# Performance work log

Measured on AMD Instinct MI355X. Metric: run time of the kernel, lower is better.

The kernel has to match this reference:

```python
import jax, jax.numpy as jnp
import numpy as np

RADIUS = 0.05      # outer ball-query radius
MIN_RADIUS = 0.02  # inner exclusion radius


def setup_inputs() -> dict:
    key = jax.random.key(0)
    k1, k2 = jax.random.split(key)
    # raw layout is [B, C, N, 1] as consumed by forward's squeeze(-1).permute(0,2,1)
    xyz = jax.random.uniform(k1, (4, 3, 4096, 1), dtype=jnp.float32)      # coords in unit cube
    points = jax.random.normal(k2, (4, 64, 4096, 1), dtype=jnp.float32)   # per-point features
    return {"xyz": xyz, "points": points}


def _pairwise_sqdist(x):
    # x: [B, N, 3] -> [B, N, N] squared euclidean distances
    sq = jnp.sum(x * x, axis=-1)  # [B, N]
    return sq[:, :, None] + sq[:, None, :] - 2.0 * jnp.einsum('bnc,bmc->bnm', x, x)


def reference(xyz, points):
    # [B, C, N, 1] -> [B, N, C]
    _xyz = jnp.transpose(xyz[..., 0], (0, 2, 1))       # [B, N, 3]
    _points = jnp.transpose(points[..., 0], (0, 2, 1))  # [B, N, D]
    B, N, C = _xyz.shape

    # downsample_query_ball: ball-query neighbor counts in annulus (min_radius, radius),
    # keep the N//2 densest points
    d2 = _pairwise_sqdist(_xyz)                              # [B, N, N]
    nbr_cnt = jnp.sum(((d2 < RADIUS ** 2) & (d2 > MIN_RADIUS ** 2)).astype(jnp.int32), axis=-1)
    _, idx = jax.lax.top_k(nbr_cnt, N // 2)                  # [B, N//2]

    # index_points: gather along the point axis
    new_xyz = jnp.take_along_axis(_xyz, idx[..., None], axis=1)        # [B, N//2, 3]
    new_points = jnp.take_along_axis(_points, idx[..., None], axis=1)  # [B, N//2, D]
    return new_xyz, new_points
```

## Files before the change

### kernel.cpp

```cpp
#include <hip/hip_runtime.h>


#define BN 4
#define NPTS 4096
#define ND 64
#define KSEL 2048
#define R2 0.0025f
#define M2 0.0004f

#define IPT 4
#define ITILES 4
#define JC 32
#define JCH 128

__global__ __launch_bounds__(256) void prep_kernel(
        const float* __restrict__ xyz, float4* __restrict__ pts4,
        int* __restrict__ counts, int* __restrict__ ranks) {
    int tid = blockIdx.x * 256 + threadIdx.x;
    int b = tid >> 12, i = tid & (NPTS - 1);
    const float* base = xyz + (size_t)b * 3 * NPTS;
    float x = base[i], y = base[NPTS + i], z = base[2 * NPTS + i];
    float sq = __fadd_rn(__fadd_rn(__fmul_rn(x, x), __fmul_rn(y, y)),
                         __fmul_rn(z, z));
    pts4[tid] = make_float4(x, y, z, sq);
    counts[tid] = 0;
    ranks[tid] = 0;
}

__global__ __launch_bounds__(256) void count_kernel(
        const float4* __restrict__ pts4, int* __restrict__ counts) {
    __shared__ float4 sj[JCH];
    const int jc = blockIdx.x & (JC - 1);
    const int it = (blockIdx.x >> 5) & (ITILES - 1);
    const int b  = blockIdx.x >> 7;
    const float4* pb = pts4 + b * NPTS;

    if (threadIdx.x < JCH) sj[threadIdx.x] = pb[jc * JCH + threadIdx.x];

    const int ibase = it * 1024 + threadIdx.x;
    float4 mi[IPT];
    #pragma unroll
    for (int k = 0; k < IPT; ++k) mi[k] = pb[ibase + k * 256];
    __syncthreads();

    int cnt[IPT] = {0, 0, 0, 0};
    #pragma unroll 2
    for (int j = 0; j < JCH; ++j) {
        float4 p = sj[j];
        #pragma unroll
        for (int k = 0; k < IPT; ++k) {
            float dot = __fadd_rn(__fadd_rn(__fmul_rn(mi[k].x, p.x),
                                            __fmul_rn(mi[k].y, p.y)),
                                  __fmul_rn(mi[k].z, p.z));
            float d2 = __fsub_rn(__fadd_rn(mi[k].w, p.w), __fmul_rn(2.0f, dot));
            cnt[k] += (d2 < R2 && d2 > M2) ? 1 : 0;
        }
    }
    #pragma unroll
    for (int k = 0; k < IPT; ++k)
        atomicAdd(&counts[b * NPTS + ibase + k * 256], cnt[k]);
}

__global__ __launch_bounds__(256) void rank_kernel(
        const int* __restrict__ counts, int* __restrict__ ranks) {
    __shared__ int skey[JCH];
    const int jc = blockIdx.x & (JC - 1);
    const int it = (blockIdx.x >> 5) & (ITILES - 1);
    const int b  = blockIdx.x >> 7;
    const int* cb = counts + b * NPTS;

    if (threadIdx.x < JCH) {
        int j = jc * JCH + threadIdx.x;
        skey[threadIdx.x] = (cb[j] << 12) | (NPTS - 1 - j);
    }
    const int ibase = it * 1024 + threadIdx.x;
    int ki[IPT];
    #pragma unroll
    for (int k = 0; k < IPT; ++k) {
        int i = ibase + k * 256;
        ki[k] = (cb[i] << 12) | (NPTS - 1 - i);
    }
    __syncthreads();

    int r[IPT] = {0, 0, 0, 0};
    #pragma unroll 2
    for (int j = 0; j < JCH; ++j) {
        int kj = skey[j];
        #pragma unroll
        for (int k = 0; k < IPT; ++k) r[k] += (kj > ki[k]) ? 1 : 0;
    }
    #pragma unroll
    for (int k = 0; k < IPT; ++k)
        atomicAdd(&ranks[b * NPTS + ibase + k * 256], r[k]);
}

__global__ __launch_bounds__(256) void scatter_kernel(
        const float4* __restrict__ pts4, const int* __restrict__ ranks,
        int* __restrict__ sel, float* __restrict__ out) {
    int tid = blockIdx.x * 256 + threadIdx.x;
    int b = tid >> 12, i = tid & (NPTS - 1);
    int r = ranks[tid];
    if (r < KSEL) {
        sel[b * KSEL + r] = i;
        float4 p = pts4[tid];
        float* o = out + (size_t)(b * KSEL + r) * 3;
        o[0] = p.x; o[1] = p.y; o[2] = p.z;
    }
}

__global__ __launch_bounds__(256) void gatherf_kernel(
        const float* __restrict__ points, const int* __restrict__ sel,
        float* __restrict__ out) {
    int flat = blockIdx.x * 256 + threadIdx.x;
    int c = flat & (ND - 1);
    int k = (flat >> 6) & (KSEL - 1);
    int b = flat >> 17;
    int i = sel[b * KSEL + k];
    out[(size_t)BN * KSEL * 3 + flat] =
        points[(size_t)(b * ND + c) * NPTS + i];
}

extern "C" void kernel_launch(void* const* d_in, const int* in_sizes, int n_in,
                              void* d_out, int out_size, void* d_ws, size_t ws_size,
                              hipStream_t stream) {
    const float* xyz    = (const float*)d_in[0];
    const float* points = (const float*)d_in[1];
    float* out = (float*)d_out;

    char* ws = (char*)d_ws;
    float4* pts4 = (float4*)ws;
    int* counts  = (int*)(ws + 256 * 1024);
    int* ranks   = (int*)(ws + 320 * 1024);
    int* sel     = (int*)(ws + 384 * 1024);

    prep_kernel<<<BN * NPTS / 256, 256, 0, stream>>>(xyz, pts4, counts, ranks);
    count_kernel<<<BN * ITILES * JC, 256, 0, stream>>>(pts4, counts);
    rank_kernel<<<BN * ITILES * JC, 256, 0, stream>>>(counts, ranks);
    scatter_kernel<<<BN * NPTS / 256, 256, 0, stream>>>(pts4, ranks, sel, out);
    gatherf_kernel<<<BN * KSEL * ND / 256, 256, 0, stream>>>(points, sel, out);
}
```

Measured before the change: 91.79 us.

## Fuse prep into counting, replace atomics with partials, fuse rank with gather

Removes the prep kernel by computing squared norms inline in the counting kernel. Per-block partial counts are written to a buffer and summed by a small key kernel, replacing atomicAdd and the zero-initialisation. The tiled rank kernel, scatter and feature gather become one kernel that holds all keys in shared memory, computes each point's rank and scatters its coordinates and features directly. This cuts five launches to three and drops the sel indirection, at the cost of only 256 blocks for the rank stage and scattered feature writes.

After: 91.43 us. Within noise of the previous version (-0.4%).

```diff
diff --git a/kernel.cpp b/kernel.cpp
--- a/kernel.cpp
+++ b/kernel.cpp
@@ -13,38 +13,35 @@
 #define JC 32
 #define JCH 128
 
-__global__ __launch_bounds__(256) void prep_kernel(
-        const float* __restrict__ xyz, float4* __restrict__ pts4,
-        int* __restrict__ counts, int* __restrict__ ranks) {
-    int tid = blockIdx.x * 256 + threadIdx.x;
-    int b = tid >> 12, i = tid & (NPTS - 1);
-    const float* base = xyz + (size_t)b * 3 * NPTS;
-    float x = base[i], y = base[NPTS + i], z = base[2 * NPTS + i];
-    float sq = __fadd_rn(__fadd_rn(__fmul_rn(x, x), __fmul_rn(y, y)),
-                         __fmul_rn(z, z));
-    pts4[tid] = make_float4(x, y, z, sq);
-    counts[tid] = 0;
-    ranks[tid] = 0;
-}
-
-__global__ __launch_bounds__(256) void count_kernel(
-        const float4* __restrict__ pts4, int* __restrict__ counts) {
+__global__ __launch_bounds__(256) void count_part_kernel(
+        const float* __restrict__ xyz, int* __restrict__ part) {
     __shared__ float4 sj[JCH];
     const int jc = blockIdx.x & (JC - 1);
     const int it = (blockIdx.x >> 5) & (ITILES - 1);
     const int b  = blockIdx.x >> 7;
-    const float4* pb = pts4 + b * NPTS;
+    const float* base = xyz + (size_t)b * 3 * NPTS;
 
-    if (threadIdx.x < JCH) sj[threadIdx.x] = pb[jc * JCH + threadIdx.x];
-
+    if (threadIdx.x < JCH) {
+        int j = jc * JCH + threadIdx.x;
+        float x = base[j], y = base[NPTS + j], z = base[2 * NPTS + j];
+        float sq = __fadd_rn(__fadd_rn(__fmul_rn(x, x), __fmul_rn(y, y)),
+                             __fmul_rn(z, z));
+        sj[threadIdx.x] = make_float4(x, y, z, sq);
+    }
     const int ibase = it * 1024 + threadIdx.x;
     float4 mi[IPT];
     #pragma unroll
-    for (int k = 0; k < IPT; ++k) mi[k] = pb[ibase + k * 256];
+    for (int k = 0; k < IPT; ++k) {
+        int i = ibase + k * 256;
+        float x = base[i], y = base[NPTS + i], z = base[2 * NPTS + i];
+        float sq = __fadd_rn(__fadd_rn(__fmul_rn(x, x), __fmul_rn(y, y)),
+                             __fmul_rn(z, z));
+        mi[k] = make_float4(x, y, z, sq);
+    }
     __syncthreads();
 
     int cnt[IPT] = {0, 0, 0, 0};
-    #pragma unroll 2
+    #pragma unroll 4
     for (int j = 0; j < JCH; ++j) {
         float4 p = sj[j];
         #pragma unroll
@@ -56,68 +53,64 @@
             cnt[k] += (d2 < R2 && d2 > M2) ? 1 : 0;
         }
     }
+    int* pp = part + (size_t)((b * ITILES + it) * JC + jc) * 1024;
     #pragma unroll
-    for (int k = 0; k < IPT; ++k)
-        atomicAdd(&counts[b * NPTS + ibase + k * 256], cnt[k]);
+    for (int k = 0; k < IPT; ++k) pp[threadIdx.x + k * 256] = cnt[k];
 }
 
-__global__ __launch_bounds__(256) void rank_kernel(
-        const int* __restrict__ counts, int* __restrict__ ranks) {
-    __shared__ int skey[JCH];
-    const int jc = blockIdx.x & (JC - 1);
-    const int it = (blockIdx.x >> 5) & (ITILES - 1);
-    const int b  = blockIdx.x >> 7;
-    const int* cb = counts + b * NPTS;
+__global__ __launch_bounds__(256) void key_kernel(
+        const int* __restrict__ part, int* __restrict__ key) {
+    int tid = blockIdx.x * 256 + threadIdx.x;
+    int b = tid >> 12, i = tid & (NPTS - 1);
+    int it = i >> 10, local = i & 1023;
+    const int* pp = part + (size_t)(b * ITILES + it) * JC * 1024 + local;
+    int c = 0;
+    #pragma unroll
+    for (int jc = 0; jc < JC; ++jc) c += pp[jc * 1024];
+    key[tid] = (c << 12) | (NPTS - 1 - i);
+}
 
-    if (threadIdx.x < JCH) {
-        int j = jc * JCH + threadIdx.x;
-        skey[threadIdx.x] = (cb[j] << 12) | (NPTS - 1 - j);
-    }
-    const int ibase = it * 1024 + threadIdx.x;
-    int ki[IPT];
-    #pragma unroll
-    for (int k = 0; k < IPT; ++k) {
-        int i = ibase + k * 256;
-        ki[k] = (cb[i] << 12) | (NPTS - 1 - i);
+__global__ __launch_bounds__(256) void rank_gather_kernel(
+        const float* __restrict__ xyz, const float* __restrict__ points,
+        const int* __restrict__ key, float* __restrict__ out) {
+    __shared__ int skey[NPTS];
+    __shared__ int spr[4][64];
+    __shared__ int srank[64];
+    const int b     = blockIdx.x >> 6;
+    const int tbase = (blockIdx.x & 63) * 64;
+    const int* kb = key + b * NPTS;
+    for (int idx = threadIdx.x; idx < NPTS; idx += 256) skey[idx] = kb[idx];
+    __syncthreads();
+
+    const int ii = threadIdx.x & 63;
+    const int q  = threadIdx.x >> 6;
+    const int ki = skey[tbase + ii];
+    int r = 0;
+    #pragma unroll 8
+    for (int j = q * 1024; j < q * 1024 + 1024; ++j)
+        r += (skey[j] > ki) ? 1 : 0;
+    spr[q][ii] = r;
+    __syncthreads();
+
+    if (threadIdx.x < 64) {
+        int rank = spr[0][threadIdx.x] + spr[1][threadIdx.x] +
+                   spr[2][threadIdx.x] + spr[3][threadIdx.x];
+        srank[threadIdx.x] = rank;
+        int i = tbase + threadIdx.x;
+        if (rank < KSEL) {
+            const float* xb = xyz + (size_t)b * 3 * NPTS;
+            float* o = out + ((size_t)b * KSEL + rank) * 3;
+            o[0] = xb[i]; o[1] = xb[NPTS + i]; o[2] = xb[2 * NPTS + i];
+        }
     }
     __syncthreads();
 
-    int r[IPT] = {0, 0, 0, 0};
-    #pragma unroll 2
-    for (int j = 0; j < JCH; ++j) {
-        int kj = skey[j];
-        #pragma unroll
-        for (int k = 0; k < IPT; ++k) r[k] += (kj > ki[k]) ? 1 : 0;
+    const int rank = srank[ii];
+    float* ofeat = out + (size_t)BN * KSEL * 3;
+    for (int c = q; c < ND; c += 4) {
+        float v = points[((size_t)b * ND + c) * NPTS + tbase + ii];
+        if (rank < KSEL) ofeat[((size_t)b * KSEL + rank) * ND + c] = v;
     }
-    #pragma unroll
-    for (int k = 0; k < IPT; ++k)
-        atomicAdd(&ranks[b * NPTS + ibase + k * 256], r[k]);
-}
-
-__global__ __launch_bounds__(256) void scatter_kernel(
-        const float4* __restrict__ pts4, const int* __restrict__ ranks,
-        int* __restrict__ sel, float* __restrict__ out) {
-    int tid = blockIdx.x * 256 + threadIdx.x;
-    int b = tid >> 12, i = tid & (NPTS - 1);
-    int r = ranks[tid];
-    if (r < KSEL) {
-        sel[b * KSEL + r] = i;
-        float4 p = pts4[tid];
-        float* o = out + (size_t)(b * KSEL + r) * 3;
-        o[0] = p.x; o[1] = p.y; o[2] = p.z;
-    }
-}
-
-__global__ __launch_bounds__(256) void gatherf_kernel(
-        const float* __restrict__ points, const int* __restrict__ sel,
-        float* __restrict__ out) {
-    int flat = blockIdx.x * 256 + threadIdx.x;
-    int c = flat & (ND - 1);
-    int k = (flat >> 6) & (KSEL - 1);
-    int b = flat >> 17;
-    int i = sel[b * KSEL + k];
-    out[(size_t)BN * KSEL * 3 + flat] =
-        points[(size_t)(b * ND + c) * NPTS + i];
 }
 
 extern "C" void kernel_launch(void* const* d_in, const int* in_sizes, int n_in,
@@ -128,14 +121,10 @@
     float* out = (float*)d_out;
 
     char* ws = (char*)d_ws;
-    float4* pts4 = (float4*)ws;
-    int* counts  = (int*)(ws + 256 * 1024);
-    int* ranks   = (int*)(ws + 320 * 1024);
-    int* sel     = (int*)(ws + 384 * 1024);
+    int* part = (int*)ws;
+    int* key  = (int*)(ws + 2 * 1024 * 1024);
 
-    prep_kernel<<<BN * NPTS / 256, 256, 0, stream>>>(xyz, pts4, counts, ranks);
-    count_kernel<<<BN * ITILES * JC, 256, 0, stream>>>(pts4, counts);
-    rank_kernel<<<BN * ITILES * JC, 256, 0, stream>>>(counts, ranks);
-    scatter_kernel<<<BN * NPTS / 256, 256, 0, stream>>>(pts4, ranks, sel, out);
-    gatherf_kernel<<<BN * KSEL * ND / 256, 256, 0, stream>>>(points, sel, out);
+    count_part_kernel<<<BN * ITILES * JC, 256, 0, stream>>>(xyz, part);
+    key_kernel<<<BN * NPTS / 256, 256, 0, stream>>>(part, key);
+    rank_gather_kernel<<<BN * 64, 256, 0, stream>>>(xyz, points, key, out);
 }
```
